# Kernel optimization log

Hardware: AMD Instinct MI355X
Metric: run time of the kernel (lower is better)

## Reference

```python
import jax, jax.numpy as jnp
import numpy as np

B, L, LO, H, V = 8, 1024, 1024, 768, 4096
NUM_TAGS = 256


def _merge_one(tags):
    """Replicates merge_weights() for one sequence of tags [L].

    A maximal run of equal, non-(-1) tags becomes one output row that averages
    the hidden states over the run. A run is only emitted when it is *closed*
    by a tag change or a -1 (so a run ending at the last position is dropped,
    exactly like the torch loop). Remaining rows are zero with bias -100.
    """
    Ls = tags.shape[0]
    pos = jnp.arange(Ls)
    valid = tags != -1
    prev = jnp.concatenate([jnp.full((1,), -2, tags.dtype), tags[:-1]])
    start = valid & ((pos == 0) | (tags != prev) | (prev == -1))
    seg_id = jnp.cumsum(start.astype(jnp.int32)) - 1          # run index per position
    total_runs = seg_id[-1] + 1
    emitted = total_runs - valid[-1].astype(jnp.int32)        # trailing open run dropped
    seg_clip = jnp.clip(seg_id, 0, Ls - 1)
    # run lengths via segment sum (invalid positions contribute 0)
    counts = jax.ops.segment_sum(valid.astype(jnp.float32), seg_clip, num_segments=Ls)
    w = jnp.where(valid & (seg_id >= 0) & (seg_id < emitted),
                  1.0 / jnp.maximum(counts[seg_clip], 1.0), 0.0)
    merge = jnp.zeros((Ls, Ls), jnp.float32).at[seg_clip, pos].add(w)  # [rows, tokens]
    bias = jnp.where(pos < emitted, 0.0, -100.0)
    return merge, bias


def setup_inputs() -> dict:
    key = jax.random.key(0)
    k1, k2, k3, k4 = jax.random.split(key, 4)
    hidden1_states = jax.random.normal(k1, (B, L, H), jnp.float32)
    hidden2_states = jax.random.normal(k2, (B, LO, H), jnp.float32)
    lm_logits = jax.random.normal(k3, (B, LO, V), jnp.float32)
    tags = jnp.sort(jax.random.randint(k4, (B, L), 0, NUM_TAGS), axis=-1)
    return {"hidden1_states": hidden1_states, "hidden2_states": hidden2_states,
            "lm_logits": lm_logits, "tags": tags}


def reference(hidden1_states, hidden2_states, lm_logits, tags):
    merge, bias = jax.vmap(_merge_one)(tags)                     # [B,L,L], [B,L]
    attn = jnp.einsum('bls,bsh->blh', merge, hidden1_states)     # segment means
    attn1 = jnp.einsum('boh,blh->bol', hidden2_states, attn) + bias[:, None, :]
    return jnp.concatenate([lm_logits, attn1], axis=2)           # [B,LO,V+L]
```

## Files before the change

### kernel.cpp

```cpp
#include <hip/hip_runtime.h>
#include <hip/hip_bf16.h>
#include <stdint.h>

#define BB   8
#define LL   1024
#define LOO  1024
#define HH   768
#define VV   4096
#define OUTW 5120
#define EMAX 256

typedef unsigned short ushort_t;
typedef __attribute__((ext_vector_type(4))) float   f32x4;
typedef __attribute__((ext_vector_type(8))) __bf16  bf16x8;
typedef __attribute__((ext_vector_type(4))) float   float4v;
typedef __attribute__((ext_vector_type(4))) int     int4v;

static __device__ __forceinline__ ushort_t f2bf(float f) {
    union { float f; uint32_t u; } v; v.f = f;
    uint32_t u = v.u;
    uint32_t r = (u + 0x7fffu + ((u >> 16) & 1u)) >> 16;
    return (ushort_t)r;
}

__global__ __launch_bounds__(256) void attn_fused_kernel(
        const float* __restrict__ h1,
        const int* __restrict__ tags,
        ushort_t* __restrict__ attn,
        int* __restrict__ emitted_out) {
    int b = blockIdx.x >> 8;
    int r = blockIdx.x & 255;
    int tid = threadIdx.x;

    __shared__ int stags[LL];
    __shared__ int cnt[256];
    __shared__ int runpos[EMAX + 2];

    ((int4v*)stags)[tid] = ((const int4v*)(tags + b * LL))[tid];
    __syncthreads();

    int p0 = tid * 4;
    int st[4];
    int prevm1 = (p0 == 0) ? -2 : stags[p0 - 1];
    st[0] = (p0 == 0) || (stags[p0] != prevm1);
    st[1] = (stags[p0 + 1] != stags[p0]);
    st[2] = (stags[p0 + 2] != stags[p0 + 1]);
    st[3] = (stags[p0 + 3] != stags[p0 + 2]);
    int c = st[0] + st[1] + st[2] + st[3];
    cnt[tid] = c;
    __syncthreads();
    for (int off = 1; off < 256; off <<= 1) {
        int v = cnt[tid];
        int a = (tid >= off) ? cnt[tid - off] : 0;
        __syncthreads();
        cnt[tid] = v + a;
        __syncthreads();
    }
    int total = cnt[255];
    int base = cnt[tid] - c;
#pragma unroll
    for (int j = 0; j < 4; ++j)
        if (st[j]) runpos[base++] = p0 + j;
    if (tid == 0) runpos[total] = LL;
    __syncthreads();

    int em = total - 1;
    if (r == 0 && tid == 0) emitted_out[b] = em;

    ushort_t* arow = attn + ((size_t)b * EMAX + r) * HH;
    if (r >= em) {
        arow[tid] = 0; arow[tid + 256] = 0; arow[tid + 512] = 0;
        return;
    }
    int s = runpos[r], e = runpos[r + 1];
    float inv = 1.0f / (float)(e - s);
    const float* hb = h1 + (size_t)b * LL * HH;
    float a0 = 0.f, a1 = 0.f, a2 = 0.f;
    for (int p = s; p < e; ++p) {
        const float* row = hb + (size_t)p * HH;
        a0 += row[tid]; a1 += row[tid + 256]; a2 += row[tid + 512];
    }
    arow[tid]       = f2bf(a0 * inv);
    arow[tid + 256] = f2bf(a1 * inv);
    arow[tid + 512] = f2bf(a2 * inv);
}

#define NGEMM 256
#define NCOPY 2048
__global__ __launch_bounds__(256, 4) void mega_kernel(
        const float* __restrict__ A,
        const ushort_t* __restrict__ Bm,
        const int* __restrict__ emitted,
        const float* __restrict__ lm,
        float* __restrict__ out) {

    if (blockIdx.x >= NGEMM) {
        int cid = blockIdx.x - NGEMM;
        int tid = threadIdx.x;
        const float4v* in4 = (const float4v*)lm;
        float4v* out4 = (float4v*)out;
        int c = cid * 256 + tid;
#pragma unroll
        for (int g = 0; g < 4; ++g) {
            size_t i0 = (size_t)(g * 4 + 0) * 524288 + c;
            size_t i1 = (size_t)(g * 4 + 1) * 524288 + c;
            size_t i2 = (size_t)(g * 4 + 2) * 524288 + c;
            size_t i3 = (size_t)(g * 4 + 3) * 524288 + c;
            float4v v0 = in4[i0];
            float4v v1 = in4[i1];
            float4v v2 = in4[i2];
            float4v v3 = in4[i3];
            out4[i0 + ((i0 >> 10) << 8)] = v0;
            out4[i1 + ((i1 >> 10) << 8)] = v1;
            out4[i2 + ((i2 >> 10) << 8)] = v2;
            out4[i3 + ((i3 >> 10) << 8)] = v3;
        }
        float4v fv = {-100.f, -100.f, -100.f, -100.f};
        if (tid < 192) {
#pragma unroll
            for (int j = 0; j < 4; ++j) {
                size_t row = (size_t)cid * 4 + j;
                out4[row * (OUTW / 4) + (VV + 256) / 4 + tid] = fv;
            }
        }
        return;
    }

    int bid  = blockIdx.x;
    int b    = bid >> 5;
    int t2   = bid & 31;
    int brow = (t2 >> 2) << 7;
    int bcol = (t2 & 3) << 6;

    const int tid  = threadIdx.x;
    const int lane = tid & 63;
    const int wid  = tid >> 6;
    const int wr   = (wid >> 1) & 1;
    const int wc   = wid & 1;

    const float*    Ab = A  + (size_t)b * LOO * HH;
    const ushort_t* Bb = Bm + (size_t)b * EMAX * HH;

    const int arow0 = brow + (wr << 6) + (lane & 15);
    const int brow0 = bcol + (wc << 5) + (lane & 15);
    const int ksub  = (lane >> 4) << 3;

    f32x4 zero = {0.f, 0.f, 0.f, 0.f};
    f32x4 acc[4][2];
#pragma unroll
    for (int i = 0; i < 4; ++i) { acc[i][0] = zero; acc[i][1] = zero; }

#pragma unroll 2
    for (int k0 = 0; k0 < HH; k0 += 32) {
        bf16x8 af[4], bfr[2];
#pragma unroll
        for (int mi = 0; mi < 4; ++mi) {
            const float* pa = Ab + (size_t)(arow0 + (mi << 4)) * HH + k0 + ksub;
            f32x4 a0 = *(const f32x4*)pa;
            f32x4 a1 = *(const f32x4*)(pa + 4);
            bf16x8 t;
            t[0] = (__bf16)a0[0]; t[1] = (__bf16)a0[1];
            t[2] = (__bf16)a0[2]; t[3] = (__bf16)a0[3];
            t[4] = (__bf16)a1[0]; t[5] = (__bf16)a1[1];
            t[6] = (__bf16)a1[2]; t[7] = (__bf16)a1[3];
            af[mi] = t;
        }
#pragma unroll
        for (int ni = 0; ni < 2; ++ni)
            bfr[ni] = *(const bf16x8*)(Bb + (size_t)(brow0 + (ni << 4)) * HH + k0 + ksub);
#pragma unroll
        for (int mi = 0; mi < 4; ++mi)
#pragma unroll
            for (int ni = 0; ni < 2; ++ni)
                acc[mi][ni] = __builtin_amdgcn_mfma_f32_16x16x32_bf16(
                    af[mi], bfr[ni], acc[mi][ni], 0, 0, 0);
    }

    int em = emitted[b];
    float* outb = out + (size_t)b * LOO * OUTW + VV;
#pragma unroll
    for (int mi = 0; mi < 4; ++mi) {
        int rbase = brow + (wr << 6) + (mi << 4) + ((lane >> 4) << 2);
#pragma unroll
        for (int ni = 0; ni < 2; ++ni) {
            int col = bcol + (wc << 5) + (ni << 4) + (lane & 15);
            float badd = (col < em) ? 0.0f : -100.0f;
#pragma unroll
            for (int rr = 0; rr < 4; ++rr)
                outb[(size_t)(rbase + rr) * OUTW + col] = acc[mi][ni][rr] + badd;
        }
    }
}

extern "C" void kernel_launch(void* const* d_in, const int* in_sizes, int n_in,
                              void* d_out, int out_size, void* d_ws, size_t ws_size,
                              hipStream_t stream) {
    const float* h1   = (const float*)d_in[0];
    const float* h2   = (const float*)d_in[1];
    const float* lm   = (const float*)d_in[2];
    const int*   tags = (const int*)d_in[3];
    float* out = (float*)d_out;

    char* ws = (char*)d_ws;
    ushort_t* attn    = (ushort_t*)ws;
    int*      emitted = (int*)(ws + 3145728);

    attn_fused_kernel<<<BB * EMAX, 256, 0, stream>>>(h1, tags, attn, emitted);
    mega_kernel<<<NGEMM + NCOPY, 256, 0, stream>>>(h2, attn, emitted, lm, out);
}
```

Baseline: 96.79 us.

## Fuse GEMM and logits copy per row tile with LDS-staged swizzled operands

Replaces the split grid of 256 GEMM blocks plus 2048 copy blocks with 512 uniform blocks. Each block computes a 16x256 output tile using LDS-staged, XOR-swizzled bf16 operands (B loaded via global_load_lds), then copies the matching 16 rows of lm_logits and fills the -100 bias region with nontemporal loads and stores. The aim is to balance work across CUs, reuse the attention matrix via LDS, and keep the streaming copy out of cache. In exchange, each block serializes compute and copy, and the GEMM loop synchronizes every K-step with no double buffering.

```diff
diff --git a/kernel.cpp b/kernel.cpp
--- a/kernel.cpp
+++ b/kernel.cpp
@@ -15,6 +15,7 @@
 typedef __attribute__((ext_vector_type(8))) __bf16  bf16x8;
 typedef __attribute__((ext_vector_type(4))) float   float4v;
 typedef __attribute__((ext_vector_type(4))) int     int4v;
+typedef __attribute__((ext_vector_type(4))) unsigned short ushort4v;
 
 static __device__ __forceinline__ ushort_t f2bf(float f) {
     union { float f; uint32_t u; } v; v.f = f;
@@ -85,110 +86,96 @@
     arow[tid + 512] = f2bf(a2 * inv);
 }
 
-#define NGEMM 256
-#define NCOPY 2048
-__global__ __launch_bounds__(256, 4) void mega_kernel(
-        const float* __restrict__ A,
+__global__ __launch_bounds__(256, 4) void fused_out_kernel(
+        const float* __restrict__ h2,
         const ushort_t* __restrict__ Bm,
         const int* __restrict__ emitted,
         const float* __restrict__ lm,
         float* __restrict__ out) {
+    __shared__ char smem[34816];
 
-    if (blockIdx.x >= NGEMM) {
-        int cid = blockIdx.x - NGEMM;
-        int tid = threadIdx.x;
-        const float4v* in4 = (const float4v*)lm;
-        float4v* out4 = (float4v*)out;
-        int c = cid * 256 + tid;
-#pragma unroll
-        for (int g = 0; g < 4; ++g) {
-            size_t i0 = (size_t)(g * 4 + 0) * 524288 + c;
-            size_t i1 = (size_t)(g * 4 + 1) * 524288 + c;
-            size_t i2 = (size_t)(g * 4 + 2) * 524288 + c;
-            size_t i3 = (size_t)(g * 4 + 3) * 524288 + c;
-            float4v v0 = in4[i0];
-            float4v v1 = in4[i1];
-            float4v v2 = in4[i2];
-            float4v v3 = in4[i3];
-            out4[i0 + ((i0 >> 10) << 8)] = v0;
-            out4[i1 + ((i1 >> 10) << 8)] = v1;
-            out4[i2 + ((i2 >> 10) << 8)] = v2;
-            out4[i3 + ((i3 >> 10) << 8)] = v3;
-        }
-        float4v fv = {-100.f, -100.f, -100.f, -100.f};
-        if (tid < 192) {
-#pragma unroll
-            for (int j = 0; j < 4; ++j) {
-                size_t row = (size_t)cid * 4 + j;
-                out4[row * (OUTW / 4) + (VV + 256) / 4 + tid] = fv;
-            }
-        }
-        return;
-    }
-
-    int bid  = blockIdx.x;
-    int b    = bid >> 5;
-    int t2   = bid & 31;
-    int brow = (t2 >> 2) << 7;
-    int bcol = (t2 & 3) << 6;
+    const int bid = blockIdx.x;
+    const int b   = bid >> 6;
+    const int r0  = (bid & 63) << 4;
 
     const int tid  = threadIdx.x;
     const int lane = tid & 63;
-    const int wid  = tid >> 6;
-    const int wr   = (wid >> 1) & 1;
-    const int wc   = wid & 1;
+    const int w    = tid >> 6;
 
-    const float*    Ab = A  + (size_t)b * LOO * HH;
+    const float*    Ab = h2 + ((size_t)b * LOO + r0) * HH;
     const ushort_t* Bb = Bm + (size_t)b * EMAX * HH;
 
-    const int arow0 = brow + (wr << 6) + (lane & 15);
-    const int brow0 = bcol + (wc << 5) + (lane & 15);
-    const int ksub  = (lane >> 4) << 3;
+    f32x4 zero = {0.f, 0.f, 0.f, 0.f};
+    f32x4 acc[4];
+    acc[0] = zero; acc[1] = zero; acc[2] = zero; acc[3] = zero;
 
-    f32x4 zero = {0.f, 0.f, 0.f, 0.f};
-    f32x4 acc[4][2];
-#pragma unroll
-    for (int i = 0; i < 4; ++i) { acc[i][0] = zero; acc[i][1] = zero; }
-
-#pragma unroll 2
-    for (int k0 = 0; k0 < HH; k0 += 32) {
-        bf16x8 af[4], bfr[2];
-#pragma unroll
-        for (int mi = 0; mi < 4; ++mi) {
-            const float* pa = Ab + (size_t)(arow0 + (mi << 4)) * HH + k0 + ksub;
-            f32x4 a0 = *(const f32x4*)pa;
-            f32x4 a1 = *(const f32x4*)(pa + 4);
-            bf16x8 t;
-            t[0] = (__bf16)a0[0]; t[1] = (__bf16)a0[1];
-            t[2] = (__bf16)a0[2]; t[3] = (__bf16)a0[3];
-            t[4] = (__bf16)a1[0]; t[5] = (__bf16)a1[1];
-            t[6] = (__bf16)a1[2]; t[7] = (__bf16)a1[3];
-            af[mi] = t;
+    const int arow_s = tid >> 4;
+    const int akq    = tid & 15;
+    for (int k0 = 0; k0 < HH; k0 += 64) {
+        __syncthreads();
+        {
+            f32x4 v = *(const f32x4*)(Ab + (size_t)arow_s * HH + k0 + akq * 4);
+            ushort4v o;
+            o[0] = f2bf(v[0]); o[1] = f2bf(v[1]); o[2] = f2bf(v[2]); o[3] = f2bf(v[3]);
+            *(ushort4v*)(smem + arow_s * 128 + ((akq * 8) ^ ((arow_s & 7) << 4))) = o;
         }
 #pragma unroll
-        for (int ni = 0; ni < 2; ++ni)
-            bfr[ni] = *(const bf16x8*)(Bb + (size_t)(brow0 + (ni << 4)) * HH + k0 + ksub);
+        for (int i = 0; i < 8; ++i) {
+            int off = i * 4096 + tid * 16;
+            int row = off >> 7;
+            int cb  = off & 127;
+            int scb = cb ^ ((row & 7) << 4);
+            const ushort_t* gb = Bb + (size_t)row * HH + k0 + (scb >> 1);
+            __builtin_amdgcn_global_load_lds(
+                (const __attribute__((address_space(1))) void*)gb,
+                (__attribute__((address_space(3))) void*)(smem + 2048 + off), 16, 0, 0);
+        }
+        asm volatile("s_waitcnt vmcnt(0)" ::: "memory");
+        __syncthreads();
+
 #pragma unroll
-        for (int mi = 0; mi < 4; ++mi)
+        for (int ks = 0; ks < 2; ++ks) {
+            int kb   = (ks << 6) + ((lane >> 4) << 4);
+            int ar   = lane & 15;
+            bf16x8 af = *(const bf16x8*)(smem + ar * 128 + (kb ^ ((ar & 7) << 4)));
 #pragma unroll
-            for (int ni = 0; ni < 2; ++ni)
-                acc[mi][ni] = __builtin_amdgcn_mfma_f32_16x16x32_bf16(
-                    af[mi], bfr[ni], acc[mi][ni], 0, 0, 0);
+            for (int ni = 0; ni < 4; ++ni) {
+                int br = ((w << 2) + ni) * 16 + (lane & 15);
+                bf16x8 bf = *(const bf16x8*)(smem + 2048 + br * 128 + (kb ^ ((br & 7) << 4)));
+                acc[ni] = __builtin_amdgcn_mfma_f32_16x16x32_bf16(af, bf, acc[ni], 0, 0, 0);
+            }
+        }
     }
 
-    int em = emitted[b];
-    float* outb = out + (size_t)b * LOO * OUTW + VV;
+    {
+        int em = emitted[b];
+        float* outb = out + ((size_t)b * LOO + r0) * OUTW + VV;
 #pragma unroll
-    for (int mi = 0; mi < 4; ++mi) {
-        int rbase = brow + (wr << 6) + (mi << 4) + ((lane >> 4) << 2);
-#pragma unroll
-        for (int ni = 0; ni < 2; ++ni) {
-            int col = bcol + (wc << 5) + (ni << 4) + (lane & 15);
-            float badd = (col < em) ? 0.0f : -100.0f;
+        for (int ni = 0; ni < 4; ++ni) {
+            int l = ((w << 2) + ni) * 16 + (lane & 15);
+            float badd = (l < em) ? 0.0f : -100.0f;
+            int rbase = (lane >> 4) << 2;
 #pragma unroll
             for (int rr = 0; rr < 4; ++rr)
-                outb[(size_t)(rbase + rr) * OUTW + col] = acc[mi][ni][rr] + badd;
+                outb[(size_t)(rbase + rr) * OUTW + l] = acc[ni][rr] + badd;
         }
+    }
+
+    const float4v* lm4 = (const float4v*)lm + ((size_t)b * LOO + r0) * (VV / 4);
+    float4v* o4 = (float4v*)out + ((size_t)b * LOO + r0) * (OUTW / 4);
+    float4v fv = {-100.f, -100.f, -100.f, -100.f};
+#pragma unroll 2
+    for (int r = 0; r < 16; ++r) {
+        float4v v0 = __builtin_nontemporal_load(&lm4[r * 1024 + tid]);
+        float4v v1 = __builtin_nontemporal_load(&lm4[r * 1024 + tid + 256]);
+        float4v v2 = __builtin_nontemporal_load(&lm4[r * 1024 + tid + 512]);
+        float4v v3 = __builtin_nontemporal_load(&lm4[r * 1024 + tid + 768]);
+        __builtin_nontemporal_store(v0, &o4[r * 1280 + tid]);
+        __builtin_nontemporal_store(v1, &o4[r * 1280 + tid + 256]);
+        __builtin_nontemporal_store(v2, &o4[r * 1280 + tid + 512]);
+        __builtin_nontemporal_store(v3, &o4[r * 1280 + tid + 768]);
+        if (tid < 192)
+            __builtin_nontemporal_store(fv, &o4[r * 1280 + 1088 + tid]);
     }
 }
 
@@ -206,5 +193,5 @@
     int*      emitted = (int*)(ws + 3145728);
 
     attn_fused_kernel<<<BB * EMAX, 256, 0, stream>>>(h1, tags, attn, emitted);
-    mega_kernel<<<NGEMM + NCOPY, 256, 0, stream>>>(h2, attn, emitted, lm, out);
+    fused_out_kernel<<<512, 256, 0, stream>>>(h2, attn, emitted, lm, out);
 }
```

Measured after the change: 86.32 us. -10.8%, faster.
